# Kernel optimization log

Measured on AMD Instinct MI355X. Metric: run time of the kernel, lower is better.

The kernel has to match this reference:

```python
import jax, jax.numpy as jnp
import numpy as np

B, T, D, H = 2, 4096, 1024, 16
DK, DV, C = 64, 128, 64  # head_k_dim, head_v_dim, chunk size


def setup_inputs() -> dict:
    key = jax.random.key(0)
    ks = jax.random.split(key, 7)
    std = 0.02
    return {
        "x": jax.random.normal(ks[0], (B, T, D), jnp.float32),
        "Wq": jax.random.normal(ks[1], (D, D), jnp.float32) * std,
        "Wk": jax.random.normal(ks[2], (D, D), jnp.float32) * std,
        "Wv": jax.random.normal(ks[3], (D, 2 * D), jnp.float32) * std,
        "Wg": jax.random.normal(ks[4], (D, 2 * D), jnp.float32) * std,
        "Wo": jax.random.normal(ks[5], (2 * D, D), jnp.float32) * std,
        "g_norm_w": jnp.ones((DV,), jnp.float32),
    }


def _rope(q, k):  # q,k: [B,T,H,DK], neox-style rotate-half rotary
    dk = q.shape[-1]
    inv = 1.0 / (10000.0 ** (jnp.arange(0, dk, 2, dtype=jnp.float32) / dk))
    t = jnp.arange(q.shape[1], dtype=jnp.float32)
    f = t[:, None] * inv[None, :]                      # [T, dk/2]
    cos = jnp.cos(f)[None, :, None, :]
    sin = jnp.sin(f)[None, :, None, :]
    def rot(x):
        x1, x2 = jnp.split(x, 2, axis=-1)
        return jnp.concatenate([x1 * cos - x2 * sin, x1 * sin + x2 * cos], -1)
    return rot(q), rot(k)


def reference(x, Wq, Wk, Wv, Wg, Wo, g_norm_w):
    b, t, _ = x.shape
    nc = t // C
    q = (x @ Wq).reshape(b, t, H, DK)
    k = (x @ Wk).reshape(b, t, H, DK)
    v = (x @ Wv).reshape(b, t, H, DV)
    g = (x @ Wg).reshape(b, t, H, DV)
    q, k = _rope(q, k)
    q = q * (DK ** -0.5)

    # per-head retention decay: gamma_h = 1 - 2^(-5-h)
    gamma = 1.0 - jnp.exp2(-5.0 - jnp.arange(H, dtype=jnp.float32))  # [H]
    i = jnp.arange(C, dtype=jnp.float32)
    dq = gamma[:, None] ** (i + 1.0)          # [H,C] cross-chunk decay on q
    dkv = gamma[:, None] ** (C - 1.0 - i)     # [H,C] decay of k into state
    rel = i[:, None] - i[None, :]
    Dmat = jnp.where(rel >= 0, gamma[:, None, None] ** jnp.maximum(rel, 0.0), 0.0)  # [H,C,C]
    gC = gamma ** C

    to_chunks = lambda a: a.reshape(b, nc, C, H, a.shape[-1]).transpose(1, 0, 3, 2, 4)
    qc, kc, vc = to_chunks(q), to_chunks(k), to_chunks(v)  # [NC,B,H,C,d]

    def step(S, inp):
        qi, ki, vi = inp
        o_inter = jnp.einsum('bhcd,bhde->bhce', qi * dq[None, :, :, None], S)
        A = jnp.einsum('bhid,bhjd->bhij', qi, ki) * Dmat[None]
        o_intra = jnp.einsum('bhij,bhje->bhie', A, vi)
        S = gC[None, :, None, None] * S + jnp.einsum('bhjd,bhje->bhde', ki * dkv[None, :, :, None], vi)
        return S, o_inter + o_intra

    S0 = jnp.zeros((b, H, DK, DV), x.dtype)
    _, o = jax.lax.scan(step, S0, (qc, kc, vc))            # [NC,B,H,C,DV]
    o = o.transpose(1, 0, 3, 2, 4).reshape(b, t, H, DV)

    # fused per-head RMSNorm + swish gate
    rms = o * jax.lax.rsqrt(jnp.mean(o * o, axis=-1, keepdims=True) + 1e-5) * g_norm_w
    o = rms * (g * jax.nn.sigmoid(g))
    return o.reshape(b, t, H * DV) @ Wo
```

## Files before the change

kernel.cpp:

```cpp
#include <hip/hip_runtime.h>
#include <stdint.h>
#include <type_traits>

typedef unsigned short u16;
typedef __attribute__((ext_vector_type(8))) short short8;
typedef __attribute__((ext_vector_type(4))) float f32x4;

#define MFMA16(a,b,c) __builtin_amdgcn_mfma_f32_16x16x32_bf16(a,b,c,0,0,0)

__device__ __forceinline__ u16 f2bf(float f){
  uint32_t u = __builtin_bit_cast(uint32_t, f);
  u += 0x7FFFu + ((u>>16)&1u);
  return (u16)(u>>16);
}
__device__ __forceinline__ float bf2f(u16 h){
  uint32_t u = ((uint32_t)h)<<16;
  return __builtin_bit_cast(float, u);
}

__global__ __launch_bounds__(256) void prep(const float* __restrict__ x, u16* __restrict__ xb,
    const float* __restrict__ Wq, const float* __restrict__ Wk, const float* __restrict__ Wv,
    const float* __restrict__ Wg, const float* __restrict__ Wo,
    u16* __restrict__ WcatT, u16* __restrict__ WoT){
  int bid = blockIdx.x;
  if (bid < 8192){
    int i = (bid*256 + threadIdx.x)*4;
    float4 v = *(const float4*)&x[i];
    uint2 u;
    u.x = (uint32_t)f2bf(v.x) | ((uint32_t)f2bf(v.y)<<16);
    u.y = (uint32_t)f2bf(v.z) | ((uint32_t)f2bf(v.w)<<16);
    *(uint2*)&xb[i] = u;
    return;
  }
  bid -= 8192;
  const float* src; u16* dst; int R, Cc, tc, tr;
  if (bid < 1024){        src=Wq; dst=WcatT;             R=1024; Cc=1024; int b=bid;      tc=(b&31)*32; tr=(b>>5)*32; }
  else if (bid < 2048){   src=Wk; dst=WcatT+1024*1024;   R=1024; Cc=1024; int b=bid-1024; tc=(b&31)*32; tr=(b>>5)*32; }
  else if (bid < 4096){   src=Wv; dst=WcatT+2048*1024;   R=1024; Cc=2048; int b=bid-2048; tc=(b&63)*32; tr=(b>>6)*32; }
  else if (bid < 6144){   src=Wg; dst=WcatT+4096*1024;   R=1024; Cc=2048; int b=bid-4096; tc=(b&63)*32; tr=(b>>6)*32; }
  else {                  src=Wo; dst=WoT;               R=2048; Cc=1024; int b=bid-6144; tc=(b&31)*32; tr=(b>>5)*32; }
  __shared__ float tile[32][33];
  int lr = threadIdx.x>>5, lc = threadIdx.x&31;
  #pragma unroll
  for (int p=0;p<4;p++)
    tile[lr+p*8][lc] = src[(size_t)(tr+lr+p*8)*Cc + tc + lc];
  __syncthreads();
  #pragma unroll
  for (int p=0;p<4;p++)
    dst[(size_t)(tc+lr+p*8)*R + tr + lc] = f2bf(tile[lc][lr+p*8]);
}

__global__ __launch_bounds__(512,1) void gemm1_256(const u16* __restrict__ A,
    const u16* __restrict__ BT, u16* __restrict__ C){
  __shared__ u16 L[4*16384];
  const int flat = blockIdx.y*24 + blockIdx.x;
  const int xcd  = flat & 7, loc = flat >> 3;
  const int bm   = xcd*4 + (loc & 3);
  const int bn   = loc >> 2;
  const int t = threadIdx.x;
  const int w = t>>6, l = t&63;
  const int wm = w>>2, wn = w&3;
  const int lr = l&15, lg = l>>4;
  const int srow = t>>2;
  const int gsw = ((t&3) - (t>>3)) & 3;
  const size_t aoff = (size_t)(bm*256 + srow)*1024 + gsw*8;
  const size_t boff = (size_t)(bn*256 + srow)*1024 + gsw*8;
  const int sdo = t*8;

  u16 *p0 = L, *p1 = L+16384, *p2 = L+32768, *p3 = L+49152;

  auto STAGE = [&](u16* buf, int k0){
    __builtin_amdgcn_global_load_lds(&A[aoff + k0],                     buf + sdo,               16,0,0);
    __builtin_amdgcn_global_load_lds(&A[aoff + (size_t)128*1024 + k0],  buf + sdo + 4096,        16,0,0);
    __builtin_amdgcn_global_load_lds(&BT[boff + k0],                    buf + 8192 + sdo,        16,0,0);
    __builtin_amdgcn_global_load_lds(&BT[boff + (size_t)128*1024 + k0], buf + 8192 + sdo + 4096, 16,0,0);
  };
  auto LDA = [&](const u16* base, int row)->short8 {
    return *(const short8*)(base + row*32 + (((lg + (row>>1))&3)<<3));
  };

  f32x4 acc[8][4];
  #pragma unroll
  for (int m=0;m<8;m++)
    #pragma unroll
    for (int n=0;n<4;n++) acc[m][n] = (f32x4){0.f,0.f,0.f,0.f};

  STAGE(p0, 0); STAGE(p1, 32); STAGE(p2, 64);
  asm volatile("s_waitcnt vmcnt(8)" ::: "memory");
  __builtin_amdgcn_s_barrier();
  short8 afA[4], afB[4], bf4[4], bf4n[4];
  #pragma unroll
  for (int m=0;m<4;m++) afA[m] = LDA(p0, wm*128 + m*16 + lr);
  #pragma unroll
  for (int n=0;n<4;n++) bf4[n] = LDA(p0 + 8192, wn*64 + n*16 + lr);

  for (int kt=0; kt<32; ++kt){
    #pragma unroll
    for (int m=0;m<4;m++) afB[m] = LDA(p0, wm*128 + (m+4)*16 + lr);
    if (kt+3 < 32) STAGE(p3, (kt+3)*32);
    __builtin_amdgcn_s_setprio(1);
    #pragma unroll
    for (int m=0;m<4;m++)
      #pragma unroll
      for (int n=0;n<4;n++)
        acc[m][n] = MFMA16(afA[m], bf4[n], acc[m][n]);
    __builtin_amdgcn_s_setprio(0);
    asm volatile("s_waitcnt lgkmcnt(0)" ::: "memory");
    __builtin_amdgcn_sched_barrier(0);
    if      (kt < 29)  asm volatile("s_waitcnt vmcnt(8)" ::: "memory");
    else if (kt == 29) asm volatile("s_waitcnt vmcnt(4)" ::: "memory");
    else               asm volatile("s_waitcnt vmcnt(0)" ::: "memory");
    __builtin_amdgcn_s_barrier();
    __builtin_amdgcn_sched_barrier(0);
    if (kt+1 < 32){
      #pragma unroll
      for (int m=0;m<4;m++) afA[m]  = LDA(p1, wm*128 + m*16 + lr);
      #pragma unroll
      for (int n=0;n<4;n++) bf4n[n] = LDA(p1 + 8192, wn*64 + n*16 + lr);
    }
    __builtin_amdgcn_s_setprio(1);
    #pragma unroll
    for (int m=0;m<4;m++)
      #pragma unroll
      for (int n=0;n<4;n++)
        acc[m+4][n] = MFMA16(afB[m], bf4[n], acc[m+4][n]);
    __builtin_amdgcn_s_setprio(0);
    if (kt+1 < 32){
      #pragma unroll
      for (int n=0;n<4;n++) bf4[n] = bf4n[n];
    }
    { u16* tp=p0; p0=p1; p1=p2; p2=p3; p3=tp; }
  }

  __syncthreads();
  const bool qk = (bn < 8);
  const float qscale = (bn < 4) ? 0.125f : 1.0f;
  #pragma unroll
  for (int s=0;s<4;++s){
    if (wm == (s>>1)){
      #pragma unroll
      for (int mm=0;mm<4;++mm){
        const int m = (s&1)*4 + mm;
        if (qk){
          #pragma unroll
          for (int n=0;n<2;n++){
            float inv = exp2f((float)(n*16+lr) * (-13.287712379549449f/32.0f));
            #pragma unroll
            for (int r=0;r<4;r++){
              int grow = bm*256 + wm*128 + m*16 + lg*4 + r;
              float f = (float)(grow & 4095) * inv;
              float sn, cs; __sincosf(f, &sn, &cs);
              float x1 = acc[m][n][r], x2 = acc[m][n+2][r];
              int lrow = mm*16 + lg*4 + r;
              L[lrow*264 + wn*64 + n*16 + lr]     = f2bf((x1*cs - x2*sn)*qscale);
              L[lrow*264 + wn*64 + (n+2)*16 + lr] = f2bf((x1*sn + x2*cs)*qscale);
            }
          }
        } else {
          #pragma unroll
          for (int n=0;n<4;n++)
            #pragma unroll
            for (int r=0;r<4;r++)
              L[(mm*16+lg*4+r)*264 + wn*64 + n*16 + lr] = f2bf(acc[m][n][r]);
        }
      }
    }
    __syncthreads();
    #pragma unroll
    for (int p=0;p<4;p++){
      int idx = p*512 + t;
      int row = idx>>5, gr = idx&31;
      *(short8*)&C[(size_t)(bm*256 + s*64 + row)*6144 + bn*256 + gr*8] =
        *(const short8*)&L[row*264 + gr*8];
    }
    __syncthreads();
  }
}

__global__ __launch_bounds__(256) void gemm2_nt(const u16* __restrict__ A,
    const u16* __restrict__ BT, float* __restrict__ C, int M, int N, int K){
  __shared__ u16 L[3*8192];
  const int flat = blockIdx.y*gridDim.x + blockIdx.x;
  const int xcd  = flat & 7, loc = flat >> 3;
  const int bm   = xcd*8 + (loc & 7);
  const int bn   = loc >> 3;
  const int t = threadIdx.x;
  const int w = t>>6, l = t&63;
  const int wr = (w>>1)*64, wc = (w&1)*64;
  const int lr = l&15, lg = l>>4;
  const int srow = t>>2;
  const int gsw  = ((t&3) - (t>>3)) & 3;
  const int scol = gsw*8;
  const size_t aoff = (size_t)(bm*128 + srow)*K + scol;
  const size_t boff = (size_t)(bn*128 + srow)*K + scol;
  const int sdo = t*8;

  u16 *a0 = L,          *b0 = L + 4096;
  u16 *a1 = L + 8192,   *b1 = L + 12288;
  u16 *a2 = L + 16384,  *b2 = L + 20480;

  auto STAGE = [&](u16* la, u16* lb, int k0){
    __builtin_amdgcn_global_load_lds(&A[aoff + k0],                 la + sdo,        16, 0, 0);
    __builtin_amdgcn_global_load_lds(&A[aoff + (size_t)64*K + k0],  la + sdo + 2048, 16, 0, 0);
    __builtin_amdgcn_global_load_lds(&BT[boff + k0],                lb + sdo,        16, 0, 0);
    __builtin_amdgcn_global_load_lds(&BT[boff + (size_t)64*K + k0], lb + sdo + 2048, 16, 0, 0);
  };

  f32x4 acc[4][4];
  for (int m=0;m<4;m++) for (int n=0;n<4;n++) acc[m][n] = (f32x4){0.f,0.f,0.f,0.f};

  const int NT = K >> 5;
  STAGE(a0, b0, 0);
  STAGE(a1, b1, 32);
  for (int kt=0; kt<NT; ++kt){
    if (kt < NT-1) asm volatile("s_waitcnt vmcnt(4)" ::: "memory");
    else           asm volatile("s_waitcnt vmcnt(0)" ::: "memory");
    __builtin_amdgcn_s_barrier();
    if (kt+2 < NT) STAGE(a2, b2, (kt+2)*32);
    short8 af[4], bfr[4];
    #pragma unroll
    for (int m=0;m<4;m++){
      int rrow = wr + m*16 + lr;
      af[m]  = *(const short8*)(a0 + rrow*32 + (((lg + (rrow>>1))&3)<<3));
    }
    #pragma unroll
    for (int n=0;n<4;n++){
      int rrow = wc + n*16 + lr;
      bfr[n] = *(const short8*)(b0 + rrow*32 + (((lg + (rrow>>1))&3)<<3));
    }
    __builtin_amdgcn_s_setprio(1);
    #pragma unroll
    for (int m=0;m<4;m++)
      #pragma unroll
      for (int n=0;n<4;n++)
        acc[m][n] = MFMA16(af[m], bfr[n], acc[m][n]);
    __builtin_amdgcn_s_setprio(0);
    { u16* tp=a0; a0=a1; a1=a2; a2=tp; }
    { u16* tp=b0; b0=b1; b1=b2; b2=tp; }
  }

  #pragma unroll
  for (int m=0;m<4;m++)
    #pragma unroll
    for (int n=0;n<4;n++){
    int row = bm*128 + wr + m*16 + lg*4;
    int col = bn*128 + wc + n*16 + lr;
    #pragma unroll
    for (int r=0;r<4;r++)
      C[(size_t)(row+r)*N + col] = acc[m][n][r];
  }
}

__global__ __launch_bounds__(256) void retention_r1(const u16* __restrict__ qkvg,
    u16* __restrict__ o, u16* __restrict__ states){
  int bid = blockIdx.x;
  int c = bid & 63, h = (bid>>6)&15, b = bid>>10;
  int t = threadIdx.x, w = t>>6, l = t&63, lr = l&15, lg = l>>4;
  __shared__ u16 SH[17280];
  __shared__ float pw[72];
  u16* kT    = SH;
  u16* vT    = SH + 4096;
  u16* A_lds = SH + 12288;
  float log2g = log2f(1.0f - exp2f(-5.0f - (float)h));
  if (t < 65) pw[t] = exp2f(log2g*(float)t);
  const size_t rowbase = (size_t)(b*4096 + c*64);
  __syncthreads();

  {
    int rp = t>>3, cg = t&7;
    int r0 = rp*2;
    short8 k0v = *(const short8*)&qkvg[(rowbase+r0  )*6144 + 1024 + h*64 + cg*8];
    short8 k1v = *(const short8*)&qkvg[(rowbase+r0+1)*6144 + 1024 + h*64 + cg*8];
    float d0 = pw[63-r0], d1 = pw[62-r0];
    #pragma unroll
    for (int j=0;j<8;j++){
      int d = cg*8+j;
      uint32_t pk = (uint32_t)f2bf(bf2f((u16)k0v[j])*d0) | ((uint32_t)f2bf(bf2f((u16)k1v[j])*d1)<<16);
      *(uint32_t*)&kT[d*64 + (((r0>>3) ^ (d>>3))<<3) + (r0&7)] = pk;
    }
    #pragma unroll
    for (int p=0;p<2;p++){
      int it = t + p*256;
      int vrp = it>>4, vcg = it&15;
      int vr0 = vrp*2;
      short8 v0 = *(const short8*)&qkvg[(rowbase+vr0  )*6144 + 2048 + h*128 + vcg*8];
      short8 v1 = *(const short8*)&qkvg[(rowbase+vr0+1)*6144 + 2048 + h*128 + vcg*8];
      #pragma unroll
      for (int j=0;j<8;j++){
        int e = vcg*8+j;
        uint32_t pv = (uint32_t)(u16)v0[j] | ((uint32_t)(u16)v1[j]<<16);
        *(uint32_t*)&vT[e*64 + (((vr0>>3) ^ ((e>>3)&7))<<3) + (vr0&7)] = pv;
      }
    }
  }

  f32x4 z4 = {0.f,0.f,0.f,0.f};
  f32x4 accA[4] = {z4,z4,z4,z4};
  #pragma unroll
  for (int ks=0;ks<2;ks++){
    short8 aq = *(const short8*)&qkvg[(rowbase + w*16+lr)*6144 + h*64 + ks*32 + lg*8];
    #pragma unroll
    for (int n=0;n<4;n++){
      short8 bk = *(const short8*)&qkvg[(rowbase + n*16+lr)*6144 + 1024 + h*64 + ks*32 + lg*8];
      accA[n] = MFMA16(aq, bk, accA[n]);
    }
  }
  #pragma unroll
  for (int n=0;n<4;n++)
    #pragma unroll
    for (int r=0;r<4;r++){
    int i = w*16 + lg*4 + r, j = n*16 + lr;
    float v = (i>=j) ? accA[n][r]*pw[i-j] : 0.0f;
    A_lds[i*72 + j] = f2bf(v);
  }
  __syncthreads();

  f32x4 accO[8], accS[8];
  #pragma unroll
  for (int n=0;n<8;n++){ accO[n]=z4; accS[n]=z4; }
  #pragma unroll
  for (int ks=0;ks<2;ks++){
    int rk = w*16+lr;
    short8 aA = *(const short8*)&A_lds[rk*72 + ks*32+lg*8];
    short8 aK = *(const short8*)&kT[rk*64 + (((ks*4+lg) ^ (rk>>3))<<3)];
    #pragma unroll
    for (int n=0;n<8;n++){
      int e2 = n*16+lr;
      short8 bv = *(const short8*)&vT[e2*64 + (((ks*4+lg) ^ ((e2>>3)&7))<<3)];
      accO[n] = MFMA16(aA, bv, accO[n]);
      accS[n] = MFMA16(aK, bv, accS[n]);
    }
  }

  __syncthreads();
  u16* oB = SH;
  u16* sB = SH + 8448;
  #pragma unroll
  for (int n=0;n<8;n++)
    #pragma unroll
    for (int r=0;r<4;r++){
    int i = w*16 + lg*4 + r, e = n*16 + lr;
    oB[i*132 + e] = f2bf(accO[n][r]);
    sB[e*68 + i]  = f2bf(accS[n][r]);
  }
  __syncthreads();
  const size_t ob = rowbase*2048 + h*128;
  const size_t sb = ((size_t)(b*16+h)*64 + c)*8192;
  {
    int orow = t>>2, ocol = (t&3)*32;
    #pragma unroll
    for (int q=0;q<4;q++)
      *(short8*)&o[ob + (size_t)orow*2048 + ocol + q*8] = *(const short8*)&oB[orow*132 + ocol + q*8];
    int se = t>>1, sd = (t&1)*32;
    #pragma unroll
    for (int q=0;q<4;q++)
      *(short8*)&states[sb + (size_t)se*64 + sd + q*8] = *(const short8*)&sB[se*68 + sd + q*8];
  }
}

__global__ __launch_bounds__(256) void retention_r2(const u16* __restrict__ qkvg,
    const u16* __restrict__ states, u16* __restrict__ o){
  int bid = blockIdx.x;
  int vblk = bid & 7, h = (bid>>3)&15, b = bid>>7;
  int t = threadIdx.x, w = t>>6, l = t&63, lr = l&15, lg = l>>4;
  int e0 = vblk*16;
  float log2g = log2f(1.0f - exp2f(-5.0f - (float)h));
  float gC = exp2f(64.0f*log2g);
  float dqv[4];
  #pragma unroll
  for (int r=0;r<4;r++) dqv[r] = exp2f(log2g*(float)(w*16 + lg*4 + r + 1));
  float st[16];
  #pragma unroll
  for (int i=0;i<16;i++) st[i]=0.f;
  const size_t sbase = ((size_t)(b*16+h)*64)*8192 + (size_t)(e0+lr)*64 + lg*8;
  const size_t qb = (size_t)(b*4096)*6144 + h*64 + (size_t)(w*16+lr)*6144 + lg*8;
  const size_t obh = (size_t)(b*4096)*2048 + h*128 + e0 + lr;
  short8 nsc0 = *(const short8*)&states[sbase];
  short8 nsc1 = *(const short8*)&states[sbase + 32];
  short8 naq0 = *(const short8*)&qkvg[qb];
  short8 naq1 = *(const short8*)&qkvg[qb + 32];
  for (int c=0;c<64;c++){
    short8 sc0 = nsc0, sc1 = nsc1, aq0 = naq0, aq1 = naq1;
    if (c < 63){
      nsc0 = *(const short8*)&states[sbase + (size_t)(c+1)*8192];
      nsc1 = *(const short8*)&states[sbase + (size_t)(c+1)*8192 + 32];
      naq0 = *(const short8*)&qkvg[qb + (size_t)(c+1)*64*6144];
      naq1 = *(const short8*)&qkvg[qb + (size_t)(c+1)*64*6144 + 32];
    }
    f32x4 acc = {0.f,0.f,0.f,0.f};
    short8 bs0, bs1;
    #pragma unroll
    for (int dd=0;dd<8;dd++) bs0[dd] = (short)f2bf(st[dd]);
    #pragma unroll
    for (int dd=0;dd<8;dd++) bs1[dd] = (short)f2bf(st[dd+8]);
    acc = MFMA16(aq0, bs0, acc);
    acc = MFMA16(aq1, bs1, acc);
    #pragma unroll
    for (int r=0;r<4;r++){
      int i = w*16 + lg*4 + r;
      size_t oi = obh + (size_t)(c*64 + i)*2048;
      o[oi] = f2bf(bf2f(o[oi]) + dqv[r]*acc[r]);
    }
    #pragma unroll
    for (int i2=0;i2<8;i2++) st[i2]   = gC*st[i2]   + bf2f((u16)sc0[i2]);
    #pragma unroll
    for (int i2=0;i2<8;i2++) st[i2+8] = gC*st[i2+8] + bf2f((u16)sc1[i2]);
  }
}

__global__ __launch_bounds__(256) void norm_gate(const u16* __restrict__ o,
    const u16* __restrict__ qkvg, const float* __restrict__ gnw, u16* __restrict__ og){
  int g16 = threadIdx.x >> 4;
  int l16 = threadIdx.x & 15;
  int rowh = blockIdx.x*16 + g16;
  int row = rowh >> 4, h = rowh & 15;
  short8 vv = *(const short8*)(o + (size_t)row*2048 + h*128 + l16*8);
  float v[8];
  float ss = 0.f;
  #pragma unroll
  for (int j=0;j<8;j++){ v[j] = bf2f((u16)vv[j]); ss += v[j]*v[j]; }
  #pragma unroll
  for (int off=8; off; off>>=1) ss += __shfl_xor(ss, off);
  float rs = rsqrtf(ss*(1.0f/128.0f) + 1e-5f);
  short8 gg = *(const short8*)(qkvg + (size_t)row*6144 + 4096 + h*128 + l16*8);
  float4 w0 = *(const float4*)&gnw[l16*8];
  float4 w1 = *(const float4*)&gnw[l16*8 + 4];
  float wv[8] = {w0.x,w0.y,w0.z,w0.w,w1.x,w1.y,w1.z,w1.w};
  short8 res;
  #pragma unroll
  for (int j=0;j<8;j++){
    float gj = bf2f((u16)gg[j]);
    float rj = v[j]*rs*wv[j] * (gj/(1.f+expf(-gj)));
    res[j] = (short)f2bf(rj);
  }
  *(short8*)(og + (size_t)row*2048 + h*128 + l16*8) = res;
}

extern "C" void kernel_launch(void* const* d_in, const int* in_sizes, int n_in,
                              void* d_out, int out_size, void* d_ws, size_t ws_size,
                              hipStream_t stream){
  const float* x   = (const float*)d_in[0];
  const float* Wq  = (const float*)d_in[1];
  const float* Wk  = (const float*)d_in[2];
  const float* Wv  = (const float*)d_in[3];
  const float* Wg  = (const float*)d_in[4];
  const float* Wo  = (const float*)d_in[5];
  const float* gnw = (const float*)d_in[6];
  float* out = (float*)d_out;

  const size_t NEED = 171966464ull;
  if (ws_size < NEED) return;

  char* base = (char*)d_ws;
  u16* qkvg  = (u16*)(base);
  u16* obuf  = (u16*)(base + 100663296);
  u16* WoT   = (u16*)(base + 134217728);
  u16* xb    = (u16*)(base + 138412032);
  u16* WcatT = (u16*)(base + 155189248);
  u16* stt   = (u16*)(base + 138412032);
  u16* og    = (u16*)(base + 138412032);

  prep<<<16384,256,0,stream>>>(x, xb, Wq, Wk, Wv, Wg, Wo, WcatT, WoT);
  gemm1_256<<<dim3(24,32),512,0,stream>>>(xb, WcatT, qkvg);
  retention_r1<<<2048,256,0,stream>>>(qkvg, obuf, stt);
  retention_r2<<<256,256,0,stream>>>(qkvg, stt, obuf);
  norm_gate<<<8192,256,0,stream>>>(obuf, qkvg, gnw, og);
  gemm2_nt<<<dim3(8,64),256,0,stream>>>(og, WoT, out, 8192, 1024, 2048);
}
```

Baseline: 287.6 us.

## Software-pipeline LDS fragment loads in GEMM and remap retention_r2 block indices

Restructures the bf16 GEMM main loop so LDS fragment reads for the next k-tile overlap with MFMAs of the current tile. The 4x4 MFMA block is split into two halves with the barrier and wait placed between them, and B fragments are double-buffered in registers. Separately, retention_r2's block-index decode is remapped so consecutive blocks share a (b,h) group differently, likely to spread blocks across XCDs or improve cache locality. This costs extra registers and relies on tighter waitcnt/barrier ordering for correctness.

```diff
diff --git a/kernel.cpp b/kernel.cpp
--- a/kernel.cpp
+++ b/kernel.cpp
@@ -205,6 +205,9 @@
     __builtin_amdgcn_global_load_lds(&BT[boff + k0],                lb + sdo,        16, 0, 0);
     __builtin_amdgcn_global_load_lds(&BT[boff + (size_t)64*K + k0], lb + sdo + 2048, 16, 0, 0);
   };
+  auto LDR = [&](const u16* base, int row)->short8 {
+    return *(const short8*)(base + row*32 + (((lg + (row>>1))&3)<<3));
+  };
 
   f32x4 acc[4][4];
   for (int m=0;m<4;m++) for (int n=0;n<4;n++) acc[m][n] = (f32x4){0.f,0.f,0.f,0.f};
@@ -212,29 +215,48 @@
   const int NT = K >> 5;
   STAGE(a0, b0, 0);
   STAGE(a1, b1, 32);
+  asm volatile("s_waitcnt vmcnt(4)" ::: "memory");
+  __builtin_amdgcn_s_barrier();
+  short8 af01[2], af23[2], bfr[4], bfrn[4];
+  #pragma unroll
+  for (int m=0;m<2;m++) af01[m] = LDR(a0, wr + m*16 + lr);
+  #pragma unroll
+  for (int n=0;n<4;n++) bfr[n] = LDR(b0, wc + n*16 + lr);
+
   for (int kt=0; kt<NT; ++kt){
-    if (kt < NT-1) asm volatile("s_waitcnt vmcnt(4)" ::: "memory");
+    #pragma unroll
+    for (int m=0;m<2;m++) af23[m] = LDR(a0, wr + (m+2)*16 + lr);
+    if (kt+2 < NT) STAGE(a2, b2, (kt+2)*32);
+    __builtin_amdgcn_s_setprio(1);
+    #pragma unroll
+    for (int m=0;m<2;m++)
+      #pragma unroll
+      for (int n=0;n<4;n++)
+        acc[m][n] = MFMA16(af01[m], bfr[n], acc[m][n]);
+    __builtin_amdgcn_s_setprio(0);
+    asm volatile("s_waitcnt lgkmcnt(0)" ::: "memory");
+    __builtin_amdgcn_sched_barrier(0);
+    if (kt < NT-2) asm volatile("s_waitcnt vmcnt(4)" ::: "memory");
     else           asm volatile("s_waitcnt vmcnt(0)" ::: "memory");
     __builtin_amdgcn_s_barrier();
-    if (kt+2 < NT) STAGE(a2, b2, (kt+2)*32);
-    short8 af[4], bfr[4];
-    #pragma unroll
-    for (int m=0;m<4;m++){
-      int rrow = wr + m*16 + lr;
-      af[m]  = *(const short8*)(a0 + rrow*32 + (((lg + (rrow>>1))&3)<<3));
-    }
-    #pragma unroll
-    for (int n=0;n<4;n++){
-      int rrow = wc + n*16 + lr;
-      bfr[n] = *(const short8*)(b0 + rrow*32 + (((lg + (rrow>>1))&3)<<3));
+    __builtin_amdgcn_sched_barrier(0);
+    if (kt+1 < NT){
+      #pragma unroll
+      for (int m=0;m<2;m++) af01[m] = LDR(a1, wr + m*16 + lr);
+      #pragma unroll
+      for (int n=0;n<4;n++) bfrn[n] = LDR(b1, wc + n*16 + lr);
     }
     __builtin_amdgcn_s_setprio(1);
     #pragma unroll
-    for (int m=0;m<4;m++)
+    for (int m=0;m<2;m++)
       #pragma unroll
       for (int n=0;n<4;n++)
-        acc[m][n] = MFMA16(af[m], bfr[n], acc[m][n]);
+        acc[m+2][n] = MFMA16(af23[m], bfr[n], acc[m+2][n]);
     __builtin_amdgcn_s_setprio(0);
+    if (kt+1 < NT){
+      #pragma unroll
+      for (int n=0;n<4;n++) bfr[n] = bfrn[n];
+    }
     { u16* tp=a0; a0=a1; a1=a2; a2=tp; }
     { u16* tp=b0; b0=b1; b1=b2; b2=tp; }
   }
@@ -361,7 +383,10 @@
 __global__ __launch_bounds__(256) void retention_r2(const u16* __restrict__ qkvg,
     const u16* __restrict__ states, u16* __restrict__ o){
   int bid = blockIdx.x;
-  int vblk = bid & 7, h = (bid>>3)&15, b = bid>>7;
+  int xq = bid & 7, qq = bid >> 3;
+  int bh = xq*4 + (qq & 3);
+  int vblk = qq >> 2;
+  int h = bh & 15, b = bh >> 4;
   int t = threadIdx.x, w = t>>6, l = t&63, lr = l&15, lg = l>>4;
   int e0 = vblk*16;
   float log2g = log2f(1.0f - exp2f(-5.0f - (float)h));
```

After: 283.2 us, median of 2. About the same (-1.5%).
